# Optimization experiments

Hardware: AMD Instinct MI355X
Metric: run time of the kernel (lower is better)

## Reference

```python
import jax, jax.numpy as jnp
import numpy as np


def _gcn_conv(x, W, b, row, col, norm, n_nodes):
    # x: [N, Fin]; W: [Fin, Fout]. PyG GCNConv: linear -> normalized gather/scatter-add -> +bias
    h = x @ W                                   # [N, Fout]
    msgs = h[row] * norm[:, None]               # [E+N, Fout] gather + scale
    out = jax.ops.segment_sum(msgs, col, num_segments=n_nodes)  # scatter-add
    return out + b


def _gcn_norm(edge_index, n_nodes):
    # add self-loops, then sym-normalize: deg^{-1/2}[row] * deg^{-1/2}[col]
    loops = jnp.arange(n_nodes, dtype=edge_index.dtype)
    row = jnp.concatenate([edge_index[0], loops])
    col = jnp.concatenate([edge_index[1], loops])
    ones = jnp.ones(row.shape[0], dtype=jnp.float32)
    deg = jax.ops.segment_sum(ones, col, num_segments=n_nodes)
    dinv = jnp.where(deg > 0, jax.lax.rsqrt(deg), 0.0)
    norm = dinv[row] * dinv[col]
    return row, col, norm


def setup_inputs() -> dict:
    key = jax.random.key(0)
    k1, k2, k3, k4 = jax.random.split(key, 4)
    N, E, F, H, C = 100000, 1600000, 256, 128, 40
    x = jax.random.normal(k1, (N, F), dtype=jnp.float32)
    edge_index = jax.random.randint(k2, (2, E), 0, N, dtype=jnp.int64)
    W1 = jax.random.normal(k3, (F, H), dtype=jnp.float32) * (1.0 / np.sqrt(F))
    b1 = jnp.zeros((H,), dtype=jnp.float32)
    W2 = jax.random.normal(k4, (H, C), dtype=jnp.float32) * (1.0 / np.sqrt(H))
    b2 = jnp.zeros((C,), dtype=jnp.float32)
    return {"x": x, "edge_index": edge_index, "W1": W1, "b1": b1, "W2": W2, "b2": b2}


def reference(x, edge_index, W1, b1, W2, b2):
    n_nodes = x.shape[0]
    row, col, norm = _gcn_norm(edge_index, n_nodes)
    h = _gcn_conv(x, W1, b1, row, col, norm, n_nodes)
    h = jax.nn.relu(h)
    # F.dropout in eval mode is identity (reference run deterministically)
    h = _gcn_conv(h, W2, b2, row, col, norm, n_nodes)
    return jax.nn.log_softmax(h, axis=1)
```

## Files before the change

kernel.cpp:

```cpp
#include <hip/hip_runtime.h>
#include <hip/hip_bf16.h>
#include <math.h>
#include <stdint.h>

typedef unsigned short u16;
typedef unsigned int u32;
typedef __attribute__((ext_vector_type(8))) short short8;
typedef __attribute__((ext_vector_type(4))) float f32x4;

#define BN 256
#define NBMAX 400
#define EPB 4096
#define ST1 160
#define ST2 192

__device__ __forceinline__ u16 bfbits(float f) {
    __hip_bfloat16 h = __float2bfloat16(f);
    return *reinterpret_cast<u16*>(&h);
}
__device__ __forceinline__ float bf2f(u16 b) {
    return __uint_as_float((uint32_t)b << 16);
}
__device__ __forceinline__ float bflo(u32 v) { return __uint_as_float(v << 16); }
__device__ __forceinline__ float bfhi(u32 v) { return __uint_as_float(v & 0xffff0000u); }

__global__ __launch_bounds__(256) void k_cnt(const int* __restrict__ col,
                                             int* __restrict__ gcnt, int E, int n, int nb) {
    __shared__ int sh[NBMAX];
    const int t = threadIdx.x;
    for (int i = t; i < nb; i += 256) sh[i] = 0;
    __syncthreads();
    const int base = blockIdx.x * EPB;
#pragma unroll
    for (int j = 0; j < 16; ++j) {
        int e = base + j * 256 + t;
        if (e < E) {
            unsigned c = (unsigned)col[e];
            if (c < (unsigned)n) atomicAdd(&sh[c >> 8], 1);
        }
    }
    __syncthreads();
    for (int i = t; i < nb; i += 256)
        if (sh[i]) atomicAdd(&gcnt[i], sh[i]);
}

__global__ __launch_bounds__(512) void k_bscan(const int* __restrict__ gcnt,
                                               int* __restrict__ ebase, int* __restrict__ cursor,
                                               int* __restrict__ off, int nb, int n) {
    __shared__ int sh[512];
    const int t = threadIdx.x;
    int v = (t < nb) ? gcnt[t] : 0;
    sh[t] = v;
    __syncthreads();
    for (int d = 1; d < 512; d <<= 1) {
        int x = (t >= d) ? sh[t - d] : 0;
        __syncthreads();
        sh[t] += x;
        __syncthreads();
    }
    if (t < nb) {
        int excl = sh[t] - v;
        ebase[t] = excl;
        cursor[t] = excl;
    }
    if (t == 0) {
        ebase[nb] = sh[511];
        off[n] = sh[511] + n;
    }
}

__global__ __launch_bounds__(256) void k_scat(const int* __restrict__ ei,
                                              int* __restrict__ cursor,
                                              u32* __restrict__ staging, int E, int n, int nb) {
    __shared__ int cnt[NBMAX];
    __shared__ int cbase[NBMAX];
    const int t = threadIdx.x;
    for (int i = t; i < nb; i += 256) cnt[i] = 0;
    __syncthreads();
    const int base = blockIdx.x * EPB;
    int rr[16], cc[16], rk[16];
#pragma unroll
    for (int j = 0; j < 16; ++j) {
        int e = base + j * 256 + t;
        cc[j] = -1;
        if (e < E) {
            unsigned r = (unsigned)ei[e], c = (unsigned)ei[E + e];
            if (r < (unsigned)n && c < (unsigned)n) {
                rr[j] = (int)r;
                cc[j] = (int)c;
                rk[j] = atomicAdd(&cnt[c >> 8], 1);
            }
        }
    }
    __syncthreads();
    for (int i = t; i < nb; i += 256)
        if (cnt[i]) cbase[i] = atomicAdd(&cursor[i], cnt[i]);
    __syncthreads();
#pragma unroll
    for (int j = 0; j < 16; ++j) {
        if (cc[j] >= 0) {
            int b = cc[j] >> 8;
            staging[cbase[b] + rk[j]] = (u32)rr[j] | ((u32)(cc[j] & (BN - 1)) << 17);
        }
    }
}

__global__ __launch_bounds__(256) void k_build(const u32* __restrict__ staging,
                                               const int* __restrict__ ebase,
                                               int* __restrict__ csrs, int* __restrict__ off,
                                               float* __restrict__ dinv, int n) {
    __shared__ int sh[256];
    __shared__ int cur[256];
    const int t = threadIdx.x;
    const int b = blockIdx.x;
    const int e0 = ebase[b], e1 = ebase[b + 1];
    const int node0 = b * BN;
    const int nn = min(BN, n - node0);
    sh[t] = 0;
    __syncthreads();
    for (int i = e0 + t; i < e1; i += 256)
        atomicAdd(&sh[staging[i] >> 17], 1);
    __syncthreads();
    const int mycnt = sh[t];
    const int myval = (t < nn) ? mycnt + 1 : 0;
    sh[t] = myval;
    __syncthreads();
    for (int d = 1; d < 256; d <<= 1) {
        int x = (t >= d) ? sh[t - d] : 0;
        __syncthreads();
        sh[t] += x;
        __syncthreads();
    }
    const int excl = sh[t] - myval;
    const int csrbase = e0 + node0;
    if (t < nn) {
        int node = node0 + t;
        int o = csrbase + excl;
        off[node] = o;
        dinv[node] = rsqrtf((float)(mycnt + 1));
        csrs[o] = node;
        cur[t] = o + 1;
    }
    __syncthreads();
    for (int i = e0 + t; i < e1; i += 256) {
        u32 v = staging[i];
        int p = atomicAdd(&cur[v >> 17], 1);
        csrs[p] = (int)(v & 0x1FFFF);
    }
}

__global__ void k_w1bf(const float* __restrict__ w1, short* __restrict__ w1bf) {
    int i = blockIdx.x * 256 + threadIdx.x;
    int e = i & 7, l = (i >> 3) & 63, kt = (i >> 9) & 7, ct = i >> 12;
    int k = kt * 32 + (l >> 4) * 8 + e;
    int c = ct * 16 + (l & 15);
    w1bf[i] = (short)bfbits(w1[(size_t)k * 128 + c]);
}

__global__ __launch_bounds__(256) void k_gemm1(const float* __restrict__ x,
                                               const short* __restrict__ w1bf,
                                               u16* __restrict__ hbf, int n) {
    const int tid = threadIdx.x;
    const int wv = tid >> 6, l = tid & 63;
    const int mrow = wv >> 1, mcol = wv & 1;
    const int lr = l & 15, kg = l >> 4;
    const int n0 = blockIdx.x * 64;

    f32x4 zero = {0.f, 0.f, 0.f, 0.f};
    f32x4 acc[2][4];
#pragma unroll
    for (int m = 0; m < 2; ++m)
#pragma unroll
        for (int c = 0; c < 4; ++c) acc[m][c] = zero;

    const float* xp[2];
#pragma unroll
    for (int m = 0; m < 2; ++m) {
        int row = n0 + 32 * mrow + 16 * m + lr;
        if (row > n - 1) row = n - 1;
        xp[m] = x + (size_t)row * 256 + kg * 8;
    }
    const short* bbase = w1bf + ((size_t)(4 * mcol) * 8) * 64 * 8 + (size_t)l * 8;

#pragma unroll 2
    for (int kt = 0; kt < 8; ++kt) {
        short8 afrag[2];
#pragma unroll
        for (int m = 0; m < 2; ++m) {
            float4 u = *(const float4*)(xp[m] + kt * 32);
            float4 v = *(const float4*)(xp[m] + kt * 32 + 4);
            short8 a;
            a[0] = (short)bfbits(u.x);
            a[1] = (short)bfbits(u.y);
            a[2] = (short)bfbits(u.z);
            a[3] = (short)bfbits(u.w);
            a[4] = (short)bfbits(v.x);
            a[5] = (short)bfbits(v.y);
            a[6] = (short)bfbits(v.z);
            a[7] = (short)bfbits(v.w);
            afrag[m] = a;
        }
#pragma unroll
        for (int c = 0; c < 4; ++c) {
            short8 bfrag = *(const short8*)(bbase + ((size_t)(c * 8 + kt) * 64) * 8);
#pragma unroll
            for (int m = 0; m < 2; ++m)
                acc[m][c] = __builtin_amdgcn_mfma_f32_16x16x32_bf16(afrag[m], bfrag,
                                                                    acc[m][c], 0, 0, 0);
        }
    }

#pragma unroll
    for (int m = 0; m < 2; ++m) {
        int rbase = n0 + 32 * mrow + 16 * m + kg * 4;
#pragma unroll
        for (int r = 0; r < 4; ++r) {
            int row = rbase + r;
            if (row < n) {
#pragma unroll
                for (int c = 0; c < 4; ++c) {
                    int col = 64 * mcol + 16 * c + lr;
                    hbf[(size_t)row * 128 + col] = bfbits(acc[m][c][r]);
                }
            }
        }
    }
}

__global__ __launch_bounds__(256) void k_agg1(const u16* __restrict__ hbf,
                                              const int* __restrict__ off,
                                              const int* __restrict__ csrs,
                                              const float* __restrict__ dinv,
                                              const float* __restrict__ b1,
                                              u16* __restrict__ h1b, int n) {
    __shared__ int s_s[4][ST1];
    __shared__ float s_f[4][ST1];
    const int t = threadIdx.x, wv = t >> 6, l = t & 63;
    const int node = blockIdx.x * 4 + wv;
    const int nd = node < n ? node : n - 1;
    const float dn = dinv[nd];
    const int e0 = off[nd], e1 = off[nd + 1];
    const int deg = e1 - e0;
    const int nst = deg < ST1 ? deg : ST1;
    for (int i = l; i < nst; i += 64) {
        int s = csrs[e0 + i];
        s_s[wv][i] = s;
        s_f[wv][i] = dinv[s] * dn;
    }
    __syncthreads();

    const u32* hb = (const u32*)hbf;
    float a0 = 0.f, a1 = 0.f;
    int i = 0;
    for (; i + 4 <= nst; i += 4) {
        int s0 = s_s[wv][i], s1 = s_s[wv][i + 1], s2 = s_s[wv][i + 2], s3 = s_s[wv][i + 3];
        float w0 = s_f[wv][i], w1 = s_f[wv][i + 1], w2v = s_f[wv][i + 2], w3 = s_f[wv][i + 3];
        u32 v0 = hb[(size_t)s0 * 64 + l];
        u32 v1 = hb[(size_t)s1 * 64 + l];
        u32 v2 = hb[(size_t)s2 * 64 + l];
        u32 v3 = hb[(size_t)s3 * 64 + l];
        a0 = fmaf(bflo(v0), w0, a0); a1 = fmaf(bfhi(v0), w0, a1);
        a0 = fmaf(bflo(v1), w1, a0); a1 = fmaf(bfhi(v1), w1, a1);
        a0 = fmaf(bflo(v2), w2v, a0); a1 = fmaf(bfhi(v2), w2v, a1);
        a0 = fmaf(bflo(v3), w3, a0); a1 = fmaf(bfhi(v3), w3, a1);
    }
    for (; i < nst; ++i) {
        int s = s_s[wv][i];
        float w = s_f[wv][i];
        u32 v = hb[(size_t)s * 64 + l];
        a0 = fmaf(bflo(v), w, a0); a1 = fmaf(bfhi(v), w, a1);
    }
    for (int j = nst; j < deg; ++j) {
        int s = csrs[e0 + j];
        float w = dinv[s] * dn;
        u32 v = hb[(size_t)s * 64 + l];
        a0 = fmaf(bflo(v), w, a0); a1 = fmaf(bfhi(v), w, a1);
    }
    float2 bb = *(const float2*)(b1 + 2 * l);
    float r0 = fmaxf(a0 + bb.x, 0.f);
    float r1 = fmaxf(a1 + bb.y, 0.f);
    if (node < n) {
        u32 o = (u32)bfbits(r0) | ((u32)bfbits(r1) << 16);
        ((u32*)h1b)[(size_t)node * 64 + l] = o;
    }
}

__global__ __launch_bounds__(64) void k_gemm2(const u16* __restrict__ h1b,
                                              const float* __restrict__ w2,
                                              u16* __restrict__ h2, int n) {
    __shared__ float hs[64 * 132];
    const int t = threadIdx.x;
    const int n0 = blockIdx.x * 64;
    const uint4* src = (const uint4*)(h1b + (size_t)n0 * 128);
#pragma unroll
    for (int i = 0; i < 16; ++i) {
        int idx = i * 64 + t;
        int r = idx >> 4, q = idx & 15;
        uint4 v = make_uint4(0u, 0u, 0u, 0u);
        if (n0 + r < n) v = src[(size_t)r * 16 + q];
        *(float4*)&hs[r * 132 + q * 8] =
            make_float4(bflo(v.x), bfhi(v.x), bflo(v.y), bfhi(v.y));
        *(float4*)&hs[r * 132 + q * 8 + 4] =
            make_float4(bflo(v.z), bfhi(v.z), bflo(v.w), bfhi(v.w));
    }
    __syncthreads();

    float acc[40];
#pragma unroll
    for (int c = 0; c < 40; ++c) acc[c] = 0.f;

    for (int k4 = 0; k4 < 32; ++k4) {
        float4 hv = *(const float4*)&hs[t * 132 + 4 * k4];
#pragma unroll
        for (int j = 0; j < 4; ++j) {
            float xv = (j == 0) ? hv.x : (j == 1) ? hv.y : (j == 2) ? hv.z : hv.w;
            const float* wr = w2 + (size_t)(4 * k4 + j) * 40;
#pragma unroll
            for (int c = 0; c < 40; ++c) acc[c] = fmaf(xv, wr[c], acc[c]);
        }
    }
    __syncthreads();
    u16* hsu = (u16*)&hs[0];
#pragma unroll
    for (int c = 0; c < 40; ++c) hsu[t * 40 + c] = bfbits(acc[c]);
    __syncthreads();
    const int lim = (n - n0 < 64 ? n - n0 : 64) * 40;
    u16* dst = h2 + (size_t)n0 * 40;
#pragma unroll
    for (int i = 0; i < 10; ++i) {
        int idx4 = i * 64 + t;
        if (idx4 * 4 < lim) {
            ushort4 v = ((const ushort4*)hsu)[idx4];
            *(ushort4*)(dst + idx4 * 4) = v;
        }
    }
}

__global__ __launch_bounds__(256) void k_agg2(const u16* __restrict__ h2,
                                              const int* __restrict__ off,
                                              const int* __restrict__ csrs,
                                              const float* __restrict__ dinv,
                                              const float* __restrict__ b2,
                                              float* __restrict__ out, int n) {
    __shared__ int s_s[4][ST2];
    __shared__ float s_f[4][ST2];
    const int t = threadIdx.x, wv = t >> 6, l = t & 63;
    const int node = blockIdx.x * 4 + wv;
    const int nd = node < n ? node : n - 1;
    const float dn = dinv[nd];
    const int e0 = off[nd], e1 = off[nd + 1];
    const int deg = e1 - e0;
    const int nst = deg < ST2 ? deg : ST2;
    for (int i = l; i < nst; i += 64) {
        int s = csrs[e0 + i];
        s_s[wv][i] = s;
        s_f[wv][i] = dinv[s] * dn;
    }
    __syncthreads();

    const int g = (l >= 40) ? 2 : (l >= 20 ? 1 : 0);
    int fl = l - 20 * g;
    if (fl > 19) fl = 19;
    const u32* hb = (const u32*)h2;

    float a0 = 0.f, a1 = 0.f;
    int base = 0;
    for (; base + 6 <= nst; base += 6) {
        int eA = base + g, eB = base + 3 + g;
        int sA = s_s[wv][eA], sB = s_s[wv][eB];
        float wA = s_f[wv][eA], wB = s_f[wv][eB];
        u32 vA = hb[(size_t)sA * 20 + fl];
        u32 vB = hb[(size_t)sB * 20 + fl];
        a0 = fmaf(bflo(vA), wA, a0); a1 = fmaf(bfhi(vA), wA, a1);
        a0 = fmaf(bflo(vB), wB, a0); a1 = fmaf(bfhi(vB), wB, a1);
    }
    for (; base < nst; base += 3) {
        int e = base + g;
        bool ok = e < nst;
        int s = ok ? s_s[wv][e] : nd;
        float w = ok ? s_f[wv][e] : 0.f;
        u32 v = hb[(size_t)s * 20 + fl];
        a0 = fmaf(bflo(v), w, a0); a1 = fmaf(bfhi(v), w, a1);
    }
    for (int j = nst; j < deg; j += 3) {
        int e = j + g;
        bool ok = e < deg;
        int s = ok ? csrs[e0 + e] : nd;
        float w = ok ? dinv[s] * dn : 0.f;
        u32 v = hb[(size_t)s * 20 + fl];
        a0 = fmaf(bflo(v), w, a0); a1 = fmaf(bfhi(v), w, a1);
    }

    float p0 = __shfl(a0, (l + 20) & 63, 64);
    float q0 = __shfl(a0, (l + 40) & 63, 64);
    float p1 = __shfl(a1, (l + 20) & 63, 64);
    float q1 = __shfl(a1, (l + 40) & 63, 64);
    float2 bb = *(const float2*)(b2 + 2 * fl);
    float v0 = a0 + p0 + q0 + bb.x;
    float v1 = a1 + p1 + q1 + bb.y;

    const bool act = (l < 20);
    float m = act ? fmaxf(v0, v1) : -INFINITY;
#pragma unroll
    for (int d = 16; d > 0; d >>= 1) m = fmaxf(m, __shfl_xor(m, d, 32));
    float s = act ? (__expf(v0 - m) + __expf(v1 - m)) : 0.f;
#pragma unroll
    for (int d = 16; d > 0; d >>= 1) s += __shfl_xor(s, d, 32);
    float ls = logf(s);
    if (node < n && act) {
        float2 o = make_float2(v0 - m - ls, v1 - m - ls);
        *(float2*)(out + (size_t)node * 40 + 2 * fl) = o;
    }
}

extern "C" void kernel_launch(void* const* d_in, const int* in_sizes, int n_in,
                              void* d_out, int out_size, void* d_ws, size_t ws_size,
                              hipStream_t stream) {
    const float* x = (const float*)d_in[0];
    const int* ei = (const int*)d_in[1];
    const float* w1 = (const float*)d_in[2];
    const float* b1 = (const float*)d_in[3];
    const float* w2 = (const float*)d_in[4];
    const float* b2 = (const float*)d_in[5];
    float* out = (float*)d_out;

    const int N = in_sizes[0] / 256;
    const int E = in_sizes[1] / 2;
    const int NB = (N + BN - 1) / BN;

    char* p = (char*)d_ws;
    auto alloc = [&](size_t bytes) {
        char* r = p;
        p += (bytes + 255) & ~(size_t)255;
        return r;
    };
    int* gcnt = (int*)alloc((size_t)NB * 4);
    int* ebase = (int*)alloc((size_t)(NB + 1) * 4);
    int* cursor = (int*)alloc((size_t)NB * 4);
    int* off = (int*)alloc((size_t)(N + 1) * 4);
    float* dinv = (float*)alloc((size_t)N * 4);
    int* csrs = (int*)alloc((size_t)(E + N) * 4);
    short* w1bf = (short*)alloc(32768 * 2);
    u16* hbf = (u16*)alloc((size_t)N * 128 * 2);
    u16* h1b = (u16*)alloc((size_t)N * 128 * 2);
    u32* staging = (u32*)h1b;
    u16* h2 = hbf;

    const int nblk = (E + EPB - 1) / EPB;

    hipMemsetAsync(gcnt, 0, (size_t)NB * 4, stream);
    k_cnt<<<nblk, 256, 0, stream>>>(ei + E, gcnt, E, N, NB);
    k_bscan<<<1, 512, 0, stream>>>(gcnt, ebase, cursor, off, NB, N);
    k_scat<<<nblk, 256, 0, stream>>>(ei, cursor, staging, E, N, NB);
    k_build<<<NB, 256, 0, stream>>>(staging, ebase, csrs, off, dinv, N);
    k_w1bf<<<128, 256, 0, stream>>>(w1, w1bf);
    k_gemm1<<<(N + 63) / 64, 256, 0, stream>>>(x, w1bf, hbf, N);
    k_agg1<<<(N + 3) / 4, 256, 0, stream>>>(hbf, off, csrs, dinv, b1, h1b, N);
    k_gemm2<<<(N + 63) / 64, 64, 0, stream>>>(h1b, w2, h2, N);
    k_agg2<<<(N + 3) / 4, 256, 0, stream>>>(h2, off, csrs, dinv, b2, out, N);
}
```

Baseline: 282.5 us.

## Store first-layer features in FP8 with permuted columns to halve gather traffic

The first GEMM now packs its output into FP8 (e4m3) with a column permutation, so each lane writes one 32-bit word per row. The first aggregation gathers 16-bit pairs of FP8 values instead of 32-bit bf16 pairs, which halves the bytes per random neighbour gather. Bias b1 and the rows of W2 are permuted to match, so the final output stays consistent. The GEMM also preloads all of its x tiles up front to overlap loads. The main risk is accuracy loss from FP8 storage of the hidden features, plus higher register pressure in the GEMM.

```diff
diff --git a/kernel.cpp b/kernel.cpp
--- a/kernel.cpp
+++ b/kernel.cpp
@@ -17,9 +17,6 @@
 __device__ __forceinline__ u16 bfbits(float f) {
     __hip_bfloat16 h = __float2bfloat16(f);
     return *reinterpret_cast<u16*>(&h);
-}
-__device__ __forceinline__ float bf2f(u16 b) {
-    return __uint_as_float((uint32_t)b << 16);
 }
 __device__ __forceinline__ float bflo(u32 v) { return __uint_as_float(v << 16); }
 __device__ __forceinline__ float bfhi(u32 v) { return __uint_as_float(v & 0xffff0000u); }
@@ -157,22 +154,30 @@
     w1bf[i] = (short)bfbits(w1[(size_t)k * 128 + c]);
 }
 
+__device__ __forceinline__ int sigma128(int col) {
+    int a = col >> 6, c = (col >> 4) & 3, lr = col & 15;
+    return (a << 6) + (lr << 2) + c;
+}
+__global__ void k_prep(const float* __restrict__ b1, const float* __restrict__ w2,
+                       float* __restrict__ b1p, float* __restrict__ w2p) {
+    int i = blockIdx.x * 256 + threadIdx.x;
+    if (i < 128) b1p[sigma128(i)] = b1[i];
+    int j = i - 128;
+    if (j >= 0 && j < 128 * 40) {
+        int col = j / 40, jj = j - col * 40;
+        w2p[sigma128(col) * 40 + jj] = w2[j];
+    }
+}
+
 __global__ __launch_bounds__(256) void k_gemm1(const float* __restrict__ x,
                                                const short* __restrict__ w1bf,
-                                               u16* __restrict__ hbf, int n) {
+                                               u32* __restrict__ hbf8, int n) {
     const int tid = threadIdx.x;
     const int wv = tid >> 6, l = tid & 63;
     const int mrow = wv >> 1, mcol = wv & 1;
     const int lr = l & 15, kg = l >> 4;
     const int n0 = blockIdx.x * 64;
 
-    f32x4 zero = {0.f, 0.f, 0.f, 0.f};
-    f32x4 acc[2][4];
-#pragma unroll
-    for (int m = 0; m < 2; ++m)
-#pragma unroll
-        for (int c = 0; c < 4; ++c) acc[m][c] = zero;
-
     const float* xp[2];
 #pragma unroll
     for (int m = 0; m < 2; ++m) {
@@ -182,13 +187,29 @@
     }
     const short* bbase = w1bf + ((size_t)(4 * mcol) * 8) * 64 * 8 + (size_t)l * 8;
 
-#pragma unroll 2
+    float4 xv[2][8][2];
+#pragma unroll
+    for (int kt = 0; kt < 8; ++kt)
+#pragma unroll
+        for (int m = 0; m < 2; ++m) {
+            xv[m][kt][0] = *(const float4*)(xp[m] + kt * 32);
+            xv[m][kt][1] = *(const float4*)(xp[m] + kt * 32 + 4);
+        }
+
+    f32x4 zero = {0.f, 0.f, 0.f, 0.f};
+    f32x4 acc[2][4];
+#pragma unroll
+    for (int m = 0; m < 2; ++m)
+#pragma unroll
+        for (int c = 0; c < 4; ++c) acc[m][c] = zero;
+
+#pragma unroll
     for (int kt = 0; kt < 8; ++kt) {
-        short8 afrag[2];
+        short8 af[2];
 #pragma unroll
         for (int m = 0; m < 2; ++m) {
-            float4 u = *(const float4*)(xp[m] + kt * 32);
-            float4 v = *(const float4*)(xp[m] + kt * 32 + 4);
+            float4 u = xv[m][kt][0];
+            float4 v = xv[m][kt][1];
             short8 a;
             a[0] = (short)bfbits(u.x);
             a[1] = (short)bfbits(u.y);
@@ -198,14 +219,14 @@
             a[5] = (short)bfbits(v.y);
             a[6] = (short)bfbits(v.z);
             a[7] = (short)bfbits(v.w);
-            afrag[m] = a;
+            af[m] = a;
         }
 #pragma unroll
         for (int c = 0; c < 4; ++c) {
             short8 bfrag = *(const short8*)(bbase + ((size_t)(c * 8 + kt) * 64) * 8);
 #pragma unroll
             for (int m = 0; m < 2; ++m)
-                acc[m][c] = __builtin_amdgcn_mfma_f32_16x16x32_bf16(afrag[m], bfrag,
+                acc[m][c] = __builtin_amdgcn_mfma_f32_16x16x32_bf16(af[m], bfrag,
                                                                     acc[m][c], 0, 0, 0);
         }
     }
@@ -217,21 +238,19 @@
         for (int r = 0; r < 4; ++r) {
             int row = rbase + r;
             if (row < n) {
-#pragma unroll
-                for (int c = 0; c < 4; ++c) {
-                    int col = 64 * mcol + 16 * c + lr;
-                    hbf[(size_t)row * 128 + col] = bfbits(acc[m][c][r]);
-                }
+                int w = __builtin_amdgcn_cvt_pk_fp8_f32(acc[m][0][r], acc[m][1][r], 0, false);
+                w = __builtin_amdgcn_cvt_pk_fp8_f32(acc[m][2][r], acc[m][3][r], w, true);
+                hbf8[(size_t)row * 32 + 16 * mcol + lr] = (u32)w;
             }
         }
     }
 }
 
-__global__ __launch_bounds__(256) void k_agg1(const u16* __restrict__ hbf,
+__global__ __launch_bounds__(256) void k_agg1(const u32* __restrict__ hbf8,
                                               const int* __restrict__ off,
                                               const int* __restrict__ csrs,
                                               const float* __restrict__ dinv,
-                                              const float* __restrict__ b1,
+                                              const float* __restrict__ b1p,
                                               u16* __restrict__ h1b, int n) {
     __shared__ int s_s[4][ST1];
     __shared__ float s_f[4][ST1];
@@ -249,7 +268,7 @@
     }
     __syncthreads();
 
-    const u32* hb = (const u32*)hbf;
+    const u16* hb = (const u16*)hbf8;
     float a0 = 0.f, a1 = 0.f;
     int i = 0;
     for (; i + 4 <= nst; i += 4) {
@@ -259,24 +278,30 @@
         u32 v1 = hb[(size_t)s1 * 64 + l];
         u32 v2 = hb[(size_t)s2 * 64 + l];
         u32 v3 = hb[(size_t)s3 * 64 + l];
-        a0 = fmaf(bflo(v0), w0, a0); a1 = fmaf(bfhi(v0), w0, a1);
-        a0 = fmaf(bflo(v1), w1, a0); a1 = fmaf(bfhi(v1), w1, a1);
-        a0 = fmaf(bflo(v2), w2v, a0); a1 = fmaf(bfhi(v2), w2v, a1);
-        a0 = fmaf(bflo(v3), w3, a0); a1 = fmaf(bfhi(v3), w3, a1);
+        a0 = fmaf(__builtin_amdgcn_cvt_f32_fp8(v0, 0), w0, a0);
+        a1 = fmaf(__builtin_amdgcn_cvt_f32_fp8(v0, 1), w0, a1);
+        a0 = fmaf(__builtin_amdgcn_cvt_f32_fp8(v1, 0), w1, a0);
+        a1 = fmaf(__builtin_amdgcn_cvt_f32_fp8(v1, 1), w1, a1);
+        a0 = fmaf(__builtin_amdgcn_cvt_f32_fp8(v2, 0), w2v, a0);
+        a1 = fmaf(__builtin_amdgcn_cvt_f32_fp8(v2, 1), w2v, a1);
+        a0 = fmaf(__builtin_amdgcn_cvt_f32_fp8(v3, 0), w3, a0);
+        a1 = fmaf(__builtin_amdgcn_cvt_f32_fp8(v3, 1), w3, a1);
     }
     for (; i < nst; ++i) {
         int s = s_s[wv][i];
         float w = s_f[wv][i];
         u32 v = hb[(size_t)s * 64 + l];
-        a0 = fmaf(bflo(v), w, a0); a1 = fmaf(bfhi(v), w, a1);
+        a0 = fmaf(__builtin_amdgcn_cvt_f32_fp8(v, 0), w, a0);
+        a1 = fmaf(__builtin_amdgcn_cvt_f32_fp8(v, 1), w, a1);
     }
     for (int j = nst; j < deg; ++j) {
         int s = csrs[e0 + j];
         float w = dinv[s] * dn;
         u32 v = hb[(size_t)s * 64 + l];
-        a0 = fmaf(bflo(v), w, a0); a1 = fmaf(bfhi(v), w, a1);
-    }
-    float2 bb = *(const float2*)(b1 + 2 * l);
+        a0 = fmaf(__builtin_amdgcn_cvt_f32_fp8(v, 0), w, a0);
+        a1 = fmaf(__builtin_amdgcn_cvt_f32_fp8(v, 1), w, a1);
+    }
+    float2 bb = *(const float2*)(b1p + 2 * l);
     float r0 = fmaxf(a0 + bb.x, 0.f);
     float r1 = fmaxf(a1 + bb.y, 0.f);
     if (node < n) {
@@ -286,7 +311,7 @@
 }
 
 __global__ __launch_bounds__(64) void k_gemm2(const u16* __restrict__ h1b,
-                                              const float* __restrict__ w2,
+                                              const float* __restrict__ w2p,
                                               u16* __restrict__ h2, int n) {
     __shared__ float hs[64 * 132];
     const int t = threadIdx.x;
@@ -314,7 +339,7 @@
 #pragma unroll
         for (int j = 0; j < 4; ++j) {
             float xv = (j == 0) ? hv.x : (j == 1) ? hv.y : (j == 2) ? hv.z : hv.w;
-            const float* wr = w2 + (size_t)(4 * k4 + j) * 40;
+            const float* wr = w2p + (size_t)(4 * k4 + j) * 40;
 #pragma unroll
             for (int c = 0; c < 40; ++c) acc[c] = fmaf(xv, wr[c], acc[c]);
         }
@@ -441,10 +466,12 @@
     float* dinv = (float*)alloc((size_t)N * 4);
     int* csrs = (int*)alloc((size_t)(E + N) * 4);
     short* w1bf = (short*)alloc(32768 * 2);
-    u16* hbf = (u16*)alloc((size_t)N * 128 * 2);
+    float* b1p = (float*)alloc(128 * 4);
+    float* w2p = (float*)alloc(128 * 40 * 4);
+    u32* hbf8 = (u32*)alloc((size_t)N * 32 * 4);
     u16* h1b = (u16*)alloc((size_t)N * 128 * 2);
     u32* staging = (u32*)h1b;
-    u16* h2 = hbf;
+    u16* h2 = (u16*)hbf8;
 
     const int nblk = (E + EPB - 1) / EPB;
 
@@ -454,8 +481,9 @@
     k_scat<<<nblk, 256, 0, stream>>>(ei, cursor, staging, E, N, NB);
     k_build<<<NB, 256, 0, stream>>>(staging, ebase, csrs, off, dinv, N);
     k_w1bf<<<128, 256, 0, stream>>>(w1, w1bf);
-    k_gemm1<<<(N + 63) / 64, 256, 0, stream>>>(x, w1bf, hbf, N);
-    k_agg1<<<(N + 3) / 4, 256, 0, stream>>>(hbf, off, csrs, dinv, b1, h1b, N);
-    k_gemm2<<<(N + 63) / 64, 64, 0, stream>>>(h1b, w2, h2, N);
+    k_prep<<<21, 256, 0, stream>>>(b1, w2, b1p, w2p);
+    k_gemm1<<<(N + 63) / 64, 256, 0, stream>>>(x, w1bf, hbf8, N);
+    k_agg1<<<(N + 3) / 4, 256, 0, stream>>>(hbf8, off, csrs, dinv, b1p, h1b, N);
+    k_gemm2<<<(N + 63) / 64, 64, 0, stream>>>(h1b, w2p, h2, N);
     k_agg2<<<(N + 3) / 4, 256, 0, stream>>>(h2, off, csrs, dinv, b2, out, N);
 }
```

Result: faster. 261.5 us (-7.4%).
